# Kernel optimization log

Measured on AMD Instinct MI355X. Metric: run time of the kernel, lower is better.

Reference implementation:

```python
import jax, jax.numpy as jnp
import numpy as np

B = 2048
H = 4096
K = 4  # conv kernel size


def setup_inputs() -> dict:
    key = jax.random.key(0)
    ks = jax.random.split(key, 9)
    s = 1.0 / np.sqrt(H)
    x = jax.random.normal(ks[0], (B, H), dtype=jnp.float32)
    conv_state = jax.random.normal(ks[1], (B, H, K - 1), dtype=jnp.float32)
    rglru_state = jax.random.normal(ks[2], (B, H), dtype=jnp.float32)
    w_fused = jax.random.uniform(ks[3], (2 * H, H), jnp.float32, -s, s)
    conv_w = jax.random.uniform(ks[4], (H, K), jnp.float32, -0.5, 0.5)
    conv_b = jax.random.uniform(ks[5], (H,), jnp.float32, -0.5, 0.5)
    w_gates = jax.random.uniform(ks[6], (2 * H, H), jnp.float32, -s, s)
    a = jax.random.uniform(ks[7], (H,), jnp.float32, 0.5, 0.9)
    w_out = jax.random.uniform(ks[8], (H, H), jnp.float32, -s, s)
    return {"x": x, "conv_state": conv_state, "rglru_state": rglru_state,
            "w_fused": w_fused, "conv_w": conv_w, "conv_b": conv_b,
            "w_gates": w_gates, "a": a, "w_out": w_out}


def reference(x, conv_state, rglru_state, w_fused, conv_w, conv_b, w_gates, a, w_out):
    # fused input projection -> gate branch + recurrent branch
    fused = x @ w_fused.T                       # [B, 2H]
    gate_out, x_recur = fused[:, :H], fused[:, H:]
    gate = jax.nn.gelu(gate_out, approximate=False)

    # single-step causal depthwise conv
    xws = jnp.concatenate([conv_state, x_recur[:, :, None]], axis=-1)  # [B, H, K]
    x_conv = jnp.einsum('bhk,hk->bh', xws, conv_w) + conv_b            # [B, H]
    new_conv_state = xws[:, :, 1:]                                     # [B, H, K-1]

    # RG-LRU gates
    gates = x_conv @ w_gates.T                  # [B, 2H]
    i_t = jax.nn.sigmoid(gates[:, :H])
    r_t = jax.nn.sigmoid(gates[:, H:])
    a_t = jnp.exp(8.0 * r_t * jnp.log(a))       # a ** (8 * r_t), a > 0
    multiplier = jnp.sqrt(1.0 - a_t * a_t)
    new_rglru_state = rglru_state * a_t + multiplier * (i_t * x_conv)

    out = (gate * new_rglru_state) @ w_out.T    # [B, H]
    return out, new_conv_state, new_rglru_state
```

## Files before the change

kernel.cpp:

```cpp
#include <hip/hip_runtime.h>
#include <cstdint>
#include <cstddef>

#define HD   4096
#define BSZ  2048

constexpr int BM = 128, BN = 128, BKT = 64;

typedef __bf16 bf16x8 __attribute__((ext_vector_type(8)));
typedef float  f32x4  __attribute__((ext_vector_type(4)));

__device__ __forceinline__ unsigned short f2bf(float f) {
  unsigned u = __float_as_uint(f);
  u += 0x7fffu + ((u >> 16) & 1u);
  return (unsigned short)(u >> 16);
}
__device__ __forceinline__ float bf2f(unsigned short s) {
  return __uint_as_float(((unsigned)s) << 16);
}

#define AS1(p) ((__attribute__((address_space(1))) void*)(void*)(p))
#define AS3(p) ((__attribute__((address_space(3))) void*)(p))

__global__ void cvt_f32_to_bf16(const float4* __restrict__ src,
                                ushort4* __restrict__ dst, int n4) {
  int i = blockIdx.x * blockDim.x + threadIdx.x;
  if (i >= n4) return;
  float4 v = src[i];
  ushort4 o;
  o.x = f2bf(v.x); o.y = f2bf(v.y); o.z = f2bf(v.z); o.w = f2bf(v.w);
  dst[i] = o;
}

template <int MODE>
__global__ __launch_bounds__(256) void gemm_bt(
    const unsigned short* __restrict__ A, const unsigned short* __restrict__ Bw,
    float* __restrict__ outf, unsigned short* __restrict__ gate_bf,
    float* __restrict__ xrec, int M, int N, int K) {
  __shared__ unsigned short smA[BM * BKT];
  __shared__ unsigned short smB[BN * BKT];
  const int tid  = threadIdx.x;
  const int wid  = tid >> 6;
  const int lane = tid & 63;
  const int wm = wid >> 1, wn = wid & 1;
  const int l16 = lane & 15, q = lane >> 4;
  const int bx = blockIdx.x, by = blockIdx.y;
  const int srow = tid >> 3;
  const int scol = (((tid & 7) ^ ((tid >> 3) & 7)) * 8);
  const unsigned short* Ab = A + (size_t)(by * BM) * K + scol;
  const unsigned short* Bb = Bw + (size_t)(bx * BN) * K + scol;
  const int ldsbase = (wid * 8) * BKT;
  f32x4 acc[4][4] = {};

  for (int kt = 0; kt < K; kt += BKT) {
#pragma unroll
    for (int i = 0; i < 4; ++i) {
      __builtin_amdgcn_global_load_lds(AS1(Ab + (size_t)(i * 32 + srow) * K + kt),
                                       AS3(smA + i * 32 * BKT + ldsbase), 16, 0, 0);
      __builtin_amdgcn_global_load_lds(AS1(Bb + (size_t)(i * 32 + srow) * K + kt),
                                       AS3(smB + i * 32 * BKT + ldsbase), 16, 0, 0);
    }
    __syncthreads();
#pragma unroll
    for (int kk = 0; kk < BKT; kk += 32) {
      bf16x8 af[4], bfr[4];
#pragma unroll
      for (int i = 0; i < 4; ++i) {
        const int ar = wm * 64 + i * 16 + l16;
        af[i]  = *(const bf16x8*)(smA + ar * BKT + ((((kk >> 3) + q) ^ (ar & 7)) * 8));
      }
#pragma unroll
      for (int j = 0; j < 4; ++j) {
        const int br = wn * 64 + j * 16 + l16;
        bfr[j] = *(const bf16x8*)(smB + br * BKT + ((((kk >> 3) + q) ^ (br & 7)) * 8));
      }
#pragma unroll
      for (int i = 0; i < 4; ++i)
#pragma unroll
        for (int j = 0; j < 4; ++j)
          acc[i][j] = __builtin_amdgcn_mfma_f32_16x16x32_bf16(af[i], bfr[j], acc[i][j], 0, 0, 0);
    }
    __syncthreads();
  }

  const int gm0 = by * BM + wm * 64 + q * 4;
  const int gn0 = bx * BN + wn * 64 + l16;
#pragma unroll
  for (int i = 0; i < 4; ++i) {
#pragma unroll
    for (int j = 0; j < 4; ++j) {
      const int n = gn0 + j * 16;
#pragma unroll
      for (int r = 0; r < 4; ++r) {
        const int m = gm0 + i * 16 + r;
        float v = acc[i][j][r];
        if (MODE == 0) {
          outf[(size_t)m * N + n] = v;
        } else if (MODE == 2) {
          float s = 1.0f / (1.0f + expf(-v));
          gate_bf[(size_t)m * N + n] = f2bf(s);
        } else {
          if (n < HD) {
            float g = 0.5f * v * (1.0f + erff(v * 0.70710678118654752f));
            gate_bf[(size_t)m * HD + n] = f2bf(g);
          } else {
            xrec[(size_t)m * HD + (n - HD)] = v;
          }
        }
      }
    }
  }
}

__device__ __forceinline__ void stage_half(const unsigned short* src_rc, int ldg,
                                           int h, int kt, unsigned short* region,
                                           int wid) {
#pragma unroll
  for (int i = 0; i < 2; ++i)
    __builtin_amdgcn_global_load_lds(
        AS1(src_rc + (size_t)(h * 128 + i * 64) * ldg + kt * 64),
        AS3(region + wid * 8 * 64 + i * 64 * 64), 16, 0, 0);
}

template <int MODE>
__global__ __launch_bounds__(512, 2) void gemm256(
    const unsigned short* __restrict__ A, const unsigned short* __restrict__ Bw,
    unsigned short* __restrict__ gate_bf, float* __restrict__ xrec,
    int N, int K) {
  __shared__ __align__(16) unsigned short sm[2][2][2][128 * 64];
  const int tid  = threadIdx.x;
  const int wid  = tid >> 6;
  const int lane = tid & 63;
  const int wm = wid >> 2, wn = wid & 3;
  const int l16 = lane & 15, q = lane >> 4;

  const int nx  = gridDim.x;
  const int lin = blockIdx.y * nx + blockIdx.x;
  const int swz = (lin & 7) * ((nx * gridDim.y) >> 3) + (lin >> 3);
  const int bx = swz % nx, by = swz / nx;

  const int srow   = tid >> 3;
  const int schunk = ((tid & 7) ^ (srow & 7)) * 8;
  const unsigned short* Asrc = A  + (size_t)(by * 256 + srow) * K + schunk;
  const unsigned short* Bsrc = Bw + (size_t)(bx * 256 + srow) * K + schunk;

  f32x4 acc[2][2][4][2] = {};
  const int NT = K >> 6;

  bf16x8 a[4][2], b0[2][2], b1[2][2];

#define BARX() __builtin_amdgcn_s_barrier()
#define LGKM0() asm volatile("s_waitcnt lgkmcnt(0)" ::: "memory")
#define READ_A(BUF, HALF)                                                      \
  {                                                                            \
    const unsigned short* rgA = &sm[BUF][0][HALF][0];                          \
    _Pragma("unroll")                                                          \
    for (int i = 0; i < 4; ++i) {                                              \
      const int r = wm * 64 + i * 16 + l16;                                    \
      const int s = r & 7;                                                     \
      a[i][0] = *(const bf16x8*)(rgA + r * 64 + ((q ^ s) << 3));               \
      a[i][1] = *(const bf16x8*)(rgA + r * 64 + (((4 + q) ^ s) << 3));         \
    }                                                                          \
  }
#define READ_B(BUF, HALF, DST)                                                 \
  {                                                                            \
    const unsigned short* rgB = &sm[BUF][1][HALF][0];                          \
    _Pragma("unroll")                                                          \
    for (int j = 0; j < 2; ++j) {                                              \
      const int r = wn * 32 + j * 16 + l16;                                    \
      const int s = r & 7;                                                     \
      DST[j][0] = *(const bf16x8*)(rgB + r * 64 + ((q ^ s) << 3));             \
      DST[j][1] = *(const bf16x8*)(rgB + r * 64 + (((4 + q) ^ s) << 3));       \
    }                                                                          \
  }
#define MFMA_Q(QA, QB, BB)                                                     \
  __builtin_amdgcn_s_setprio(1);                                               \
  _Pragma("unroll")                                                            \
  for (int i = 0; i < 4; ++i)                                                  \
    _Pragma("unroll")                                                          \
    for (int j = 0; j < 2; ++j) {                                              \
      acc[QA][QB][i][j] = __builtin_amdgcn_mfma_f32_16x16x32_bf16(             \
          a[i][0], BB[j][0], acc[QA][QB][i][j], 0, 0, 0);                      \
      acc[QA][QB][i][j] = __builtin_amdgcn_mfma_f32_16x16x32_bf16(             \
          a[i][1], BB[j][1], acc[QA][QB][i][j], 0, 0, 0);                      \
    }                                                                          \
  __builtin_amdgcn_s_setprio(0)

  stage_half(Asrc, K, 0, 0, &sm[0][0][0][0], wid);
  stage_half(Bsrc, K, 0, 0, &sm[0][1][0][0], wid);
  stage_half(Bsrc, K, 1, 0, &sm[0][1][1][0], wid);
  stage_half(Asrc, K, 1, 0, &sm[0][0][1][0], wid);
  stage_half(Asrc, K, 0, 1, &sm[1][0][0][0], wid);
  stage_half(Bsrc, K, 0, 1, &sm[1][1][0][0], wid);
  stage_half(Bsrc, K, 1, 1, &sm[1][1][1][0], wid);
  asm volatile("s_waitcnt vmcnt(6)" ::: "memory");
  BARX();

  for (int it = 0; it < (NT >> 1); ++it) {
    const int t1 = 2 * it + 1, t2 = 2 * it + 2, t3 = 2 * it + 3;
    READ_A(0, 0); READ_B(0, 0, b0);
    stage_half(Asrc, K, 1, t1, &sm[1][0][1][0], wid);
    BARX(); LGKM0();
    MFMA_Q(0, 0, b0);
    BARX();
    READ_B(0, 1, b1);
    if (t2 < NT) stage_half(Asrc, K, 0, t2, &sm[0][0][0][0], wid);
    BARX(); LGKM0();
    MFMA_Q(0, 1, b1);
    BARX();
    READ_A(0, 1);
    if (t2 < NT) stage_half(Bsrc, K, 0, t2, &sm[0][1][0][0], wid);
    BARX(); LGKM0();
    MFMA_Q(1, 0, b0);
    BARX();
    if (t2 < NT) {
      stage_half(Bsrc, K, 1, t2, &sm[0][1][1][0], wid);
      asm volatile("s_waitcnt vmcnt(6)" ::: "memory");
    } else {
      asm volatile("s_waitcnt vmcnt(0)" ::: "memory");
    }
    BARX();
    MFMA_Q(1, 1, b1);
    BARX();
    READ_A(1, 0); READ_B(1, 0, b0);
    if (t2 < NT) stage_half(Asrc, K, 1, t2, &sm[0][0][1][0], wid);
    BARX(); LGKM0();
    MFMA_Q(0, 0, b0);
    BARX();
    READ_B(1, 1, b1);
    if (t3 < NT) stage_half(Asrc, K, 0, t3, &sm[1][0][0][0], wid);
    BARX(); LGKM0();
    MFMA_Q(0, 1, b1);
    BARX();
    READ_A(1, 1);
    if (t3 < NT) stage_half(Bsrc, K, 0, t3, &sm[1][1][0][0], wid);
    BARX(); LGKM0();
    MFMA_Q(1, 0, b0);
    BARX();
    if (t3 < NT) {
      stage_half(Bsrc, K, 1, t3, &sm[1][1][1][0], wid);
      asm volatile("s_waitcnt vmcnt(6)" ::: "memory");
    } else {
      asm volatile("s_waitcnt vmcnt(0)" ::: "memory");
    }
    BARX();
    MFMA_Q(1, 1, b1);
    BARX();
  }
#undef MFMA_Q
#undef READ_B
#undef READ_A
#undef LGKM0
#undef BARX

  const int m0 = by * 256 + wm * 64 + q * 4;
  const int n0 = bx * 256 + wn * 32 + l16;
#pragma unroll
  for (int qa = 0; qa < 2; ++qa)
#pragma unroll
    for (int qb = 0; qb < 2; ++qb)
#pragma unroll
      for (int i = 0; i < 4; ++i)
#pragma unroll
        for (int j = 0; j < 2; ++j)
#pragma unroll
          for (int r = 0; r < 4; ++r) {
            const int m = m0 + qa * 128 + i * 16 + r;
            const int n = n0 + qb * 128 + j * 16;
            float v = acc[qa][qb][i][j][r];
            if (MODE == 2) {
              gate_bf[(size_t)m * N + n] = f2bf(1.0f / (1.0f + expf(-v)));
            } else {
              if (n < HD) {
                float g = 0.5f * v * (1.0f + erff(v * 0.70710678118654752f));
                gate_bf[(size_t)m * HD + n] = f2bf(g);
              } else {
                xrec[(size_t)m * HD + (n - HD)] = v;
              }
            }
          }
}

__global__ void conv_fuse(const float* __restrict__ cs, const float* xr,
                          const float4* __restrict__ cw, const float* __restrict__ cb,
                          float* __restrict__ ncs, float* xc_out,
                          unsigned short* __restrict__ xc_bf) {
  int t = blockIdx.x * 256 + threadIdx.x;
  int h = t & (HD - 1);
  float c0 = cs[3 * t + 0];
  float c1 = cs[3 * t + 1];
  float c2 = cs[3 * t + 2];
  float xv = xr[t];
  float4 w = cw[h];
  float v = fmaf(c0, w.x, fmaf(c1, w.y, fmaf(c2, w.z, fmaf(xv, w.w, cb[h]))));
  ncs[3 * t + 0] = c1;
  ncs[3 * t + 1] = c2;
  ncs[3 * t + 2] = xv;
  xc_out[t] = v;
  xc_bf[t] = f2bf(v);
}

__global__ void rglru_fuse(const unsigned short* __restrict__ gates_bf,
                           const float* __restrict__ av,
                           const float* __restrict__ rs, const float* __restrict__ xc,
                           const unsigned short* __restrict__ gbf,
                           float* __restrict__ nrs, unsigned short* __restrict__ gated) {
  int t = blockIdx.x * 256 + threadIdx.x;
  int h = t & (HD - 1);
  int b = t >> 12;
  float it = bf2f(gates_bf[(size_t)b * (2 * HD) + h]);
  float rt = bf2f(gates_bf[(size_t)b * (2 * HD) + HD + h]);
  float at = expf(8.0f * rt * logf(av[h]));
  float mult = sqrtf(fmaxf(0.0f, 1.0f - at * at));
  float x = xc[t];
  float nv = fmaf(rs[t], at, mult * (it * x));
  nrs[t] = nv;
  gated[t] = f2bf(bf2f(gbf[t]) * nv);
}

extern "C" void kernel_launch(void* const* d_in, const int* in_sizes, int n_in,
                              void* d_out, int out_size, void* d_ws, size_t ws_size,
                              hipStream_t stream) {
  const float* x  = (const float*)d_in[0];
  const float* cs = (const float*)d_in[1];
  const float* rs = (const float*)d_in[2];
  const float* wf = (const float*)d_in[3];
  const float* cw = (const float*)d_in[4];
  const float* cb = (const float*)d_in[5];
  const float* wg = (const float*)d_in[6];
  const float* av = (const float*)d_in[7];
  const float* wo = (const float*)d_in[8];

  float* out = (float*)d_out;
  float* ncs = out + (size_t)BSZ * HD;
  float* nrs = out + (size_t)BSZ * HD * 4;

  char* ws = (char*)d_ws;
  unsigned short* x_bf   = (unsigned short*)(ws);
  unsigned short* wf_bf  = (unsigned short*)(ws + (size_t)(16u)  * 1048576u);
  unsigned short* wg_bf  = (unsigned short*)(ws + (size_t)(80u)  * 1048576u);
  unsigned short* wo_bf  = (unsigned short*)(ws + (size_t)(144u) * 1048576u);
  unsigned short* gatebf = (unsigned short*)(ws + (size_t)(176u) * 1048576u);
  float*          xrc    = (float*)         (ws + (size_t)(192u) * 1048576u);
  unsigned short* xc_bf  = (unsigned short*)(ws + (size_t)(224u) * 1048576u);
  unsigned short* gates_bf = wf_bf;
  unsigned short* gated    = x_bf;

  cvt_f32_to_bf16<<<(BSZ * HD / 4) / 256, 256, 0, stream>>>((const float4*)x,  (ushort4*)x_bf,  BSZ * HD / 4);
  cvt_f32_to_bf16<<<(2 * HD * HD / 4) / 256, 256, 0, stream>>>((const float4*)wf, (ushort4*)wf_bf, 2 * HD * HD / 4);
  cvt_f32_to_bf16<<<(2 * HD * HD / 4) / 256, 256, 0, stream>>>((const float4*)wg, (ushort4*)wg_bf, 2 * HD * HD / 4);
  cvt_f32_to_bf16<<<(HD * HD / 4) / 256, 256, 0, stream>>>((const float4*)wo, (ushort4*)wo_bf, HD * HD / 4);

  dim3 g256(2 * HD / 256, BSZ / 256);
  gemm256<1><<<g256, 512, 0, stream>>>(x_bf, wf_bf, gatebf, xrc, 2 * HD, HD);
  conv_fuse<<<(BSZ * HD) / 256, 256, 0, stream>>>(cs, xrc, (const float4*)cw, cb, ncs, xrc, xc_bf);
  gemm256<2><<<g256, 512, 0, stream>>>(xc_bf, wg_bf, gates_bf, nullptr, 2 * HD, HD);
  rglru_fuse<<<(BSZ * HD) / 256, 256, 0, stream>>>(gates_bf, av, rs, xrc, gatebf, nrs, gated);
  dim3 g3(HD / BN, BSZ / BM);
  gemm_bt<0><<<g3, dim3(256), 0, stream>>>(gated, wo_bf, out, nullptr, nullptr, BSZ, HD, HD);
}
```

Measured before the change: 884.6 us.

## Merge conversion kernels, constant-fold GEMM dims, peel last K iteration, remap XCD tiles

```diff
diff --git a/kernel.cpp b/kernel.cpp
--- a/kernel.cpp
+++ b/kernel.cpp
@@ -22,21 +22,31 @@
 #define AS1(p) ((__attribute__((address_space(1))) void*)(void*)(p))
 #define AS3(p) ((__attribute__((address_space(3))) void*)(p))
 
-__global__ void cvt_f32_to_bf16(const float4* __restrict__ src,
-                                ushort4* __restrict__ dst, int n4) {
-  int i = blockIdx.x * blockDim.x + threadIdx.x;
-  if (i >= n4) return;
-  float4 v = src[i];
-  ushort4 o;
-  o.x = f2bf(v.x); o.y = f2bf(v.y); o.z = f2bf(v.z); o.w = f2bf(v.w);
-  dst[i] = o;
-}
-
-template <int MODE>
+__global__ void cvt_all(const float4* __restrict__ x,  const float4* __restrict__ wf,
+                        const float4* __restrict__ wg, const float4* __restrict__ wo,
+                        ushort4* __restrict__ xb,  ushort4* __restrict__ wfb,
+                        ushort4* __restrict__ wgb, ushort4* __restrict__ wob) {
+  constexpr int NX = BSZ * HD / 4;
+  constexpr int NW = 2 * HD * HD / 4;
+  constexpr int NO = HD * HD / 4;
+  int i = blockIdx.x * 256 + threadIdx.x;
+  const float4* s; ushort4* d; int o;
+  if (i < NX)               { s = x;  d = xb;  o = i; }
+  else if (i < NX + NW)     { s = wf; d = wfb; o = i - NX; }
+  else if (i < NX + 2 * NW) { s = wg; d = wgb; o = i - (NX + NW); }
+  else                      { s = wo; d = wob; o = i - (NX + 2 * NW); }
+  float4 v = s[o];
+  ushort4 r;
+  r.x = f2bf(v.x); r.y = f2bf(v.y); r.z = f2bf(v.z); r.w = f2bf(v.w);
+  d[o] = r;
+  (void)NO;
+}
+
+template <int MODE, int NN, int KK>
 __global__ __launch_bounds__(256) void gemm_bt(
     const unsigned short* __restrict__ A, const unsigned short* __restrict__ Bw,
     float* __restrict__ outf, unsigned short* __restrict__ gate_bf,
-    float* __restrict__ xrec, int M, int N, int K) {
+    float* __restrict__ xrec) {
   __shared__ unsigned short smA[BM * BKT];
   __shared__ unsigned short smB[BN * BKT];
   const int tid  = threadIdx.x;
@@ -47,17 +57,17 @@
   const int bx = blockIdx.x, by = blockIdx.y;
   const int srow = tid >> 3;
   const int scol = (((tid & 7) ^ ((tid >> 3) & 7)) * 8);
-  const unsigned short* Ab = A + (size_t)(by * BM) * K + scol;
-  const unsigned short* Bb = Bw + (size_t)(bx * BN) * K + scol;
+  const unsigned short* Ab = A + (size_t)(by * BM) * KK + scol;
+  const unsigned short* Bb = Bw + (size_t)(bx * BN) * KK + scol;
   const int ldsbase = (wid * 8) * BKT;
   f32x4 acc[4][4] = {};
 
-  for (int kt = 0; kt < K; kt += BKT) {
+  for (int kt = 0; kt < KK; kt += BKT) {
 #pragma unroll
     for (int i = 0; i < 4; ++i) {
-      __builtin_amdgcn_global_load_lds(AS1(Ab + (size_t)(i * 32 + srow) * K + kt),
+      __builtin_amdgcn_global_load_lds(AS1(Ab + (size_t)(i * 32 + srow) * KK + kt),
                                        AS3(smA + i * 32 * BKT + ldsbase), 16, 0, 0);
-      __builtin_amdgcn_global_load_lds(AS1(Bb + (size_t)(i * 32 + srow) * K + kt),
+      __builtin_amdgcn_global_load_lds(AS1(Bb + (size_t)(i * 32 + srow) * KK + kt),
                                        AS3(smB + i * 32 * BKT + ldsbase), 16, 0, 0);
     }
     __syncthreads();
@@ -95,10 +105,10 @@
         const int m = gm0 + i * 16 + r;
         float v = acc[i][j][r];
         if (MODE == 0) {
-          outf[(size_t)m * N + n] = v;
+          outf[(size_t)m * NN + n] = v;
         } else if (MODE == 2) {
           float s = 1.0f / (1.0f + expf(-v));
-          gate_bf[(size_t)m * N + n] = f2bf(s);
+          gate_bf[(size_t)m * NN + n] = f2bf(s);
         } else {
           if (n < HD) {
             float g = 0.5f * v * (1.0f + erff(v * 0.70710678118654752f));
@@ -112,48 +122,47 @@
   }
 }
 
-__device__ __forceinline__ void stage_half(const unsigned short* src_rc, int ldg,
-                                           int h, int kt, unsigned short* region,
-                                           int wid) {
+__device__ __forceinline__ void stage_half4(const unsigned short* src_rc,
+                                            int h, int t,
+                                            unsigned short* region, int wid) {
 #pragma unroll
   for (int i = 0; i < 2; ++i)
     __builtin_amdgcn_global_load_lds(
-        AS1(src_rc + (size_t)(h * 128 + i * 64) * ldg + kt * 64),
+        AS1(src_rc + (size_t)(h * 128 + i * 64) * HD + t * 64),
         AS3(region + wid * 8 * 64 + i * 64 * 64), 16, 0, 0);
 }
 
-template <int MODE>
-__global__ __launch_bounds__(512, 2) void gemm256(
+__global__ __launch_bounds__(512, 2) void gemm256_k(
     const unsigned short* __restrict__ A, const unsigned short* __restrict__ Bw,
     unsigned short* __restrict__ gate_bf, float* __restrict__ xrec,
-    int N, int K) {
-  __shared__ __align__(16) unsigned short sm[2][2][2][128 * 64];
+    const int MODE) {
+  __shared__ __align__(16) unsigned short smA[2][2][8192];
+  __shared__ __align__(16) unsigned short smB[2][2][8192];
   const int tid  = threadIdx.x;
   const int wid  = tid >> 6;
   const int lane = tid & 63;
   const int wm = wid >> 2, wn = wid & 3;
   const int l16 = lane & 15, q = lane >> 4;
-
-  const int nx  = gridDim.x;
-  const int lin = blockIdx.y * nx + blockIdx.x;
-  const int swz = (lin & 7) * ((nx * gridDim.y) >> 3) + (lin >> 3);
-  const int bx = swz % nx, by = swz / nx;
+  constexpr int NN = 2 * HD;
+  constexpr int NT = HD / 64;
+
+  const int lin = blockIdx.y * 32 + blockIdx.x;
+  const int xcd = lin & 7, idx = lin >> 3;
+  const int bx = xcd * 4 + (idx & 3), by = idx >> 2;
 
   const int srow   = tid >> 3;
   const int schunk = ((tid & 7) ^ (srow & 7)) * 8;
-  const unsigned short* Asrc = A  + (size_t)(by * 256 + srow) * K + schunk;
-  const unsigned short* Bsrc = Bw + (size_t)(bx * 256 + srow) * K + schunk;
+  const unsigned short* Asrc = A  + (size_t)(by * 256 + srow) * HD + schunk;
+  const unsigned short* Bsrc = Bw + (size_t)(bx * 256 + srow) * HD + schunk;
 
   f32x4 acc[2][2][4][2] = {};
-  const int NT = K >> 6;
-
   bf16x8 a[4][2], b0[2][2], b1[2][2];
 
 #define BARX() __builtin_amdgcn_s_barrier()
 #define LGKM0() asm volatile("s_waitcnt lgkmcnt(0)" ::: "memory")
 #define READ_A(BUF, HALF)                                                      \
   {                                                                            \
-    const unsigned short* rgA = &sm[BUF][0][HALF][0];                          \
+    const unsigned short* rgA = &smA[BUF][HALF][0];                            \
     _Pragma("unroll")                                                          \
     for (int i = 0; i < 4; ++i) {                                              \
       const int r = wm * 64 + i * 16 + l16;                                    \
@@ -164,7 +173,7 @@
   }
 #define READ_B(BUF, HALF, DST)                                                 \
   {                                                                            \
-    const unsigned short* rgB = &sm[BUF][1][HALF][0];                          \
+    const unsigned short* rgB = &smB[BUF][HALF][0];                            \
     _Pragma("unroll")                                                          \
     for (int j = 0; j < 2; ++j) {                                              \
       const int r = wn * 32 + j * 16 + l16;                                    \
@@ -186,67 +195,68 @@
     }                                                                          \
   __builtin_amdgcn_s_setprio(0)
 
-  stage_half(Asrc, K, 0, 0, &sm[0][0][0][0], wid);
-  stage_half(Bsrc, K, 0, 0, &sm[0][1][0][0], wid);
-  stage_half(Bsrc, K, 1, 0, &sm[0][1][1][0], wid);
-  stage_half(Asrc, K, 1, 0, &sm[0][0][1][0], wid);
-  stage_half(Asrc, K, 0, 1, &sm[1][0][0][0], wid);
-  stage_half(Bsrc, K, 0, 1, &sm[1][1][0][0], wid);
-  stage_half(Bsrc, K, 1, 1, &sm[1][1][1][0], wid);
+#define KITER(T0, D2, D3)                                                      \
+  {                                                                            \
+    const int t1 = (T0) + 1, t2 = (T0) + 2, t3 = (T0) + 3;                     \
+                                      \
+    READ_A(0, 0); READ_B(0, 0, b0);                                            \
+    stage_half4(Asrc, 1, t1, &smA[1][1][0], wid);                              \
+    asm volatile("s_waitcnt lgkmcnt(8)" ::: "memory");                         \
+    BARX(); LGKM0(); MFMA_Q(0, 0, b0); BARX();                                 \
+                                         \
+    READ_B(0, 1, b1);                                                          \
+    if (D2) stage_half4(Asrc, 0, t2, &smA[0][0][0], wid);                      \
+    BARX(); LGKM0(); MFMA_Q(0, 1, b1); BARX();                                 \
+                                         \
+    READ_A(0, 1);                                                              \
+    if (D2) stage_half4(Bsrc, 0, t2, &smB[0][0][0], wid);                      \
+    BARX(); LGKM0(); MFMA_Q(1, 0, b0); BARX();                                 \
+                                     \
+    if (D2) {                                                                  \
+      stage_half4(Bsrc, 1, t2, &smB[0][1][0], wid);                            \
+      asm volatile("s_waitcnt vmcnt(6)" ::: "memory");                         \
+    } else {                                                                   \
+      asm volatile("s_waitcnt vmcnt(0)" ::: "memory");                         \
+    }                                                                          \
+    BARX(); MFMA_Q(1, 1, b1); BARX();                                          \
+                                      \
+    READ_A(1, 0); READ_B(1, 0, b0);                                            \
+    if (D2) stage_half4(Asrc, 1, t2, &smA[0][1][0], wid);                      \
+    asm volatile("s_waitcnt lgkmcnt(8)" ::: "memory");                         \
+    BARX(); LGKM0(); MFMA_Q(0, 0, b0); BARX();                                 \
+                                         \
+    READ_B(1, 1, b1);                                                          \
+    if (D3) stage_half4(Asrc, 0, t3, &smA[1][0][0], wid);                      \
+    BARX(); LGKM0(); MFMA_Q(0, 1, b1); BARX();                                 \
+                                         \
+    READ_A(1, 1);                                                              \
+    if (D3) stage_half4(Bsrc, 0, t3, &smB[1][0][0], wid);                      \
+    BARX(); LGKM0(); MFMA_Q(1, 0, b0); BARX();                                 \
+                                     \
+    if (D3) {                                                                  \
+      stage_half4(Bsrc, 1, t3, &smB[1][1][0], wid);                            \
+      asm volatile("s_waitcnt vmcnt(6)" ::: "memory");                         \
+    } else {                                                                   \
+      asm volatile("s_waitcnt vmcnt(0)" ::: "memory");                         \
+    }                                                                          \
+    BARX(); MFMA_Q(1, 1, b1); BARX();                                          \
+  }
+
+  stage_half4(Asrc, 0, 0, &smA[0][0][0], wid);
+  stage_half4(Bsrc, 0, 0, &smB[0][0][0], wid);
+  stage_half4(Bsrc, 1, 0, &smB[0][1][0], wid);
+  stage_half4(Asrc, 1, 0, &smA[0][1][0], wid);
+  stage_half4(Asrc, 0, 1, &smA[1][0][0], wid);
+  stage_half4(Bsrc, 0, 1, &smB[1][0][0], wid);
+  stage_half4(Bsrc, 1, 1, &smB[1][1][0], wid);
   asm volatile("s_waitcnt vmcnt(6)" ::: "memory");
   BARX();
 
-  for (int it = 0; it < (NT >> 1); ++it) {
-    const int t1 = 2 * it + 1, t2 = 2 * it + 2, t3 = 2 * it + 3;
-    READ_A(0, 0); READ_B(0, 0, b0);
-    stage_half(Asrc, K, 1, t1, &sm[1][0][1][0], wid);
-    BARX(); LGKM0();
-    MFMA_Q(0, 0, b0);
-    BARX();
-    READ_B(0, 1, b1);
-    if (t2 < NT) stage_half(Asrc, K, 0, t2, &sm[0][0][0][0], wid);
-    BARX(); LGKM0();
-    MFMA_Q(0, 1, b1);
-    BARX();
-    READ_A(0, 1);
-    if (t2 < NT) stage_half(Bsrc, K, 0, t2, &sm[0][1][0][0], wid);
-    BARX(); LGKM0();
-    MFMA_Q(1, 0, b0);
-    BARX();
-    if (t2 < NT) {
-      stage_half(Bsrc, K, 1, t2, &sm[0][1][1][0], wid);
-      asm volatile("s_waitcnt vmcnt(6)" ::: "memory");
-    } else {
-      asm volatile("s_waitcnt vmcnt(0)" ::: "memory");
-    }
-    BARX();
-    MFMA_Q(1, 1, b1);
-    BARX();
-    READ_A(1, 0); READ_B(1, 0, b0);
-    if (t2 < NT) stage_half(Asrc, K, 1, t2, &sm[0][0][1][0], wid);
-    BARX(); LGKM0();
-    MFMA_Q(0, 0, b0);
-    BARX();
-    READ_B(1, 1, b1);
-    if (t3 < NT) stage_half(Asrc, K, 0, t3, &sm[1][0][0][0], wid);
-    BARX(); LGKM0();
-    MFMA_Q(0, 1, b1);
-    BARX();
-    READ_A(1, 1);
-    if (t3 < NT) stage_half(Bsrc, K, 0, t3, &sm[1][1][0][0], wid);
-    BARX(); LGKM0();
-    MFMA_Q(1, 0, b0);
-    BARX();
-    if (t3 < NT) {
-      stage_half(Bsrc, K, 1, t3, &sm[1][1][1][0], wid);
-      asm volatile("s_waitcnt vmcnt(6)" ::: "memory");
-    } else {
-      asm volatile("s_waitcnt vmcnt(0)" ::: "memory");
-    }
-    BARX();
-    MFMA_Q(1, 1, b1);
-    BARX();
-  }
+#pragma unroll 1
+  for (int it = 0; it < (NT >> 1) - 1; ++it) KITER(2 * it, true, true);
+  KITER(NT - 2, false, false);
+
+#undef KITER
 #undef MFMA_Q
 #undef READ_B
 #undef READ_A
@@ -269,7 +279,7 @@
             const int n = n0 + qb * 128 + j * 16;
             float v = acc[qa][qb][i][j][r];
             if (MODE == 2) {
-              gate_bf[(size_t)m * N + n] = f2bf(1.0f / (1.0f + expf(-v)));
+              gate_bf[(size_t)m * NN + n] = f2bf(1.0f / (1.0f + expf(-v)));
             } else {
               if (n < HD) {
                 float g = 0.5f * v * (1.0f + erff(v * 0.70710678118654752f));
@@ -346,16 +356,16 @@
   unsigned short* gates_bf = wf_bf;
   unsigned short* gated    = x_bf;
 
-  cvt_f32_to_bf16<<<(BSZ * HD / 4) / 256, 256, 0, stream>>>((const float4*)x,  (ushort4*)x_bf,  BSZ * HD / 4);
-  cvt_f32_to_bf16<<<(2 * HD * HD / 4) / 256, 256, 0, stream>>>((const float4*)wf, (ushort4*)wf_bf, 2 * HD * HD / 4);
-  cvt_f32_to_bf16<<<(2 * HD * HD / 4) / 256, 256, 0, stream>>>((const float4*)wg, (ushort4*)wg_bf, 2 * HD * HD / 4);
-  cvt_f32_to_bf16<<<(HD * HD / 4) / 256, 256, 0, stream>>>((const float4*)wo, (ushort4*)wo_bf, HD * HD / 4);
+  constexpr int CVT_BLKS = (BSZ * HD / 4 + 2 * (2 * HD * HD / 4) + HD * HD / 4) / 256;
+  cvt_all<<<CVT_BLKS, 256, 0, stream>>>(
+      (const float4*)x, (const float4*)wf, (const float4*)wg, (const float4*)wo,
+      (ushort4*)x_bf, (ushort4*)wf_bf, (ushort4*)wg_bf, (ushort4*)wo_bf);
 
   dim3 g256(2 * HD / 256, BSZ / 256);
-  gemm256<1><<<g256, 512, 0, stream>>>(x_bf, wf_bf, gatebf, xrc, 2 * HD, HD);
+  gemm256_k<<<g256, 512, 0, stream>>>(x_bf, wf_bf, gatebf, xrc, 1);
   conv_fuse<<<(BSZ * HD) / 256, 256, 0, stream>>>(cs, xrc, (const float4*)cw, cb, ncs, xrc, xc_bf);
-  gemm256<2><<<g256, 512, 0, stream>>>(xc_bf, wg_bf, gates_bf, nullptr, 2 * HD, HD);
+  gemm256_k<<<g256, 512, 0, stream>>>(xc_bf, wg_bf, gates_bf, nullptr, 2);
   rglru_fuse<<<(BSZ * HD) / 256, 256, 0, stream>>>(gates_bf, av, rs, xrc, gatebf, nrs, gated);
   dim3 g3(HD / BN, BSZ / BM);
-  gemm_bt<0><<<g3, dim3(256), 0, stream>>>(gated, wo_bf, out, nullptr, nullptr, BSZ, HD, HD);
-}
+  gemm_bt<0, HD, HD><<<g3, dim3(256), 0, stream>>>(gated, wo_bf, out, nullptr, nullptr);
+}
```

Measured after the change: 905.2 us. 1.02x slower.
